# Kernel tuning notes

Hardware: AMD Instinct MI355X
Metric: run time of the kernel (lower is better)

Reference implementation:

```python
import jax, jax.numpy as jnp
import numpy as np

D_MODEL = 1024
EXPAND = 2
HEADDIM = 64
D_STATE = 128
D_CONV = 4
D_INNER = EXPAND * D_MODEL          # 2048
NHEADS = D_INNER // HEADDIM         # 32
CONV_DIM = D_INNER + 2 * D_STATE    # x, B, C share the depthwise conv
EPS = 1e-5


def setup_inputs() -> dict:
    key = jax.random.key(0)
    ks = jax.random.split(key, 8)
    d_in_proj = 2 * D_INNER + 2 * D_STATE + NHEADS
    x = jax.random.normal(ks[0], (2, 2048, D_MODEL), jnp.float32)
    W_in = jax.random.normal(ks[1], (D_MODEL, d_in_proj), jnp.float32) * (D_MODEL ** -0.5)
    conv_w = jax.random.normal(ks[2], (CONV_DIM, D_CONV), jnp.float32) * 0.2
    conv_b = jnp.zeros((CONV_DIM,), jnp.float32)
    # dt init: softplus(dt_bias) in [1e-3, 1e-1]  (inverse-softplus init, as in mamba_ssm)
    dt = jnp.exp(jax.random.uniform(ks[3], (NHEADS,), jnp.float32,
                                    minval=np.log(1e-3), maxval=np.log(1e-1)))
    dt_bias = dt + jnp.log(-jnp.expm1(-dt))
    A_log = jnp.log(jax.random.uniform(ks[4], (NHEADS,), jnp.float32, minval=1.0, maxval=16.0))
    D = jnp.ones((NHEADS,), jnp.float32)
    norm_w = jnp.ones((D_INNER,), jnp.float32)
    W_out = jax.random.normal(ks[5], (D_INNER, D_MODEL), jnp.float32) * (D_INNER ** -0.5)
    return dict(x=x, W_in=W_in, conv_w=conv_w, conv_b=conv_b, dt_bias=dt_bias,
                A_log=A_log, D=D, norm_w=norm_w, W_out=W_out)


def _causal_depthwise_conv(u, w, b):
    # u: (B, L, C), w: (C, K) depthwise, causal (pad K-1 on the left)
    B, L, C = u.shape
    up = jnp.pad(u, ((0, 0), (D_CONV - 1, 0), (0, 0)))
    y = b
    for k in range(D_CONV):
        y = y + up[:, k:k + L, :] * w[:, k]
    return y


def _rms(v):
    return v * jax.lax.rsqrt(jnp.mean(v * v, axis=-1, keepdims=True) + EPS)


def reference(x, W_in, conv_w, conv_b, dt_bias, A_log, D, norm_w, W_out):
    b, l, _ = x.shape
    zxbcdt = x @ W_in                                  # (b, l, 2*d_inner + 2*d_state + nheads)
    z = zxbcdt[..., :D_INNER]
    xBC = zxbcdt[..., D_INNER:D_INNER + CONV_DIM]
    dt = jax.nn.softplus(zxbcdt[..., -NHEADS:] + dt_bias)   # (b, l, h)
    xBC = jax.nn.silu(_causal_depthwise_conv(xBC, conv_w, conv_b))
    xs = xBC[..., :D_INNER].reshape(b, l, NHEADS, HEADDIM)  # (b, l, h, p)
    Bm = xBC[..., D_INNER:D_INNER + D_STATE]                 # (b, l, n)
    Cm = xBC[..., D_INNER + D_STATE:]                        # (b, l, n)
    A = -jnp.exp(A_log)                                      # (h,)
    decay = jnp.exp(dt * A)                                  # (b, l, h)

    def step(h, inp):
        dec_t, dt_t, x_t, B_t, C_t = inp   # (b,h) (b,h) (b,h,p) (b,n) (b,n)
        h = h * dec_t[:, :, None, None] + (dt_t[:, :, None] * x_t)[..., None] * B_t[:, None, None, :]
        y_t = jnp.einsum('bhpn,bn->bhp', h, C_t)
        return h, y_t

    h0 = jnp.zeros((b, NHEADS, HEADDIM, D_STATE), x.dtype)
    xs_t = (decay.transpose(1, 0, 2), dt.transpose(1, 0, 2),
            xs.transpose(1, 0, 2, 3), Bm.transpose(1, 0, 2), Cm.transpose(1, 0, 2))
    _, ys = jax.lax.scan(step, h0, xs_t)                     # ys: (l, b, h, p)
    y = ys.transpose(1, 0, 2, 3) + D[None, None, :, None] * xs
    y = y.reshape(b, l, D_INNER)
    # gated RMSNorm (RMSNormGated in mamba_ssm), then out projection
    y = _rms(y * jax.nn.silu(z)) * norm_w
    out = y @ W_out                                          # (b, l, d_model)
    # wrapper: post RMSNorm (weight freshly initialized to ones) + residual
    return _rms(out) + x
```

## Files before the change

### kernel.cpp

```cpp
#include <hip/hip_runtime.h>
#include <hip/hip_bf16.h>

#define DMODEL 1024
#define DI     2048
#define DSTATE 128
#define NH     32
#define HD     64
#define CONVD  2304
#define LSEQ   2048
#define BATCH  2
#define DPROJ  4384
#define NPAD   4480
#define EPSV   1e-5f
#define QCH    128
#define NCH    16

#define AS1 __attribute__((address_space(1)))
#define AS3 __attribute__((address_space(3)))

typedef __attribute__((ext_vector_type(8))) short bf16x8;
typedef __attribute__((ext_vector_type(4))) float f32x4;

union U4 { ushort4 u; __hip_bfloat16 h[4]; };

__device__ __forceinline__ float bf2f(unsigned short u) {
  union { unsigned int i; float f; } c; c.i = ((unsigned)u) << 16; return c.f;
}
__device__ __forceinline__ ushort4 pack4(float x0, float x1, float x2, float x3) {
  U4 p;
  p.h[0] = __float2bfloat16(x0); p.h[1] = __float2bfloat16(x1);
  p.h[2] = __float2bfloat16(x2); p.h[3] = __float2bfloat16(x3);
  return p.u;
}

__device__ __forceinline__ bf16x8 ldsfrag(const __hip_bfloat16* base, int row, int ke) {
  int byte = row * 256 + ke * 2;
  byte ^= (row & 7) << 4;
  return *reinterpret_cast<const bf16x8*>(reinterpret_cast<const char*>(base) + byte);
}
__device__ __forceinline__ void ldswr4(__hip_bfloat16* base, int row, int col, ushort4 v) {
  int byte = row * 256 + col * 2;
  byte ^= (row & 7) << 4;
  *reinterpret_cast<ushort4*>(reinterpret_cast<char*>(base) + byte) = v;
}
__device__ __forceinline__ ushort4 ldsrd4(const __hip_bfloat16* base, int row, int col) {
  int byte = row * 256 + col * 2;
  byte ^= (row & 7) << 4;
  return *reinterpret_cast<const ushort4*>(reinterpret_cast<const char*>(base) + byte);
}
__device__ __forceinline__ void ldswr8(__hip_bfloat16* base, int row, int colElem,
                                       unsigned lo, unsigned hi) {
  int byte = row * 256 + colElem * 2;
  byte ^= (row & 7) << 4;
  uint2 v; v.x = lo; v.y = hi;
  *reinterpret_cast<uint2*>(reinterpret_cast<char*>(base) + byte) = v;
}
__device__ __forceinline__ bf16x8 frag32(const __hip_bfloat16* base, int row, int g) {
  int byte = row * 64 + (((g ^ (row >> 1)) & 3) << 4);
  return *reinterpret_cast<const bf16x8*>(reinterpret_cast<const char*>(base) + byte);
}

__device__ __forceinline__ void quadtr(unsigned a01, unsigned a23, int ql,
                                       unsigned& w01, unsigned& w23) {
  unsigned y01 = __shfl_xor((int)a01, 1), y23 = __shfl_xor((int)a23, 1);
  unsigned c01 = (ql & 1) ? ((y01 >> 16) | (a01 & 0xFFFF0000u))
                          : ((a01 & 0xFFFFu) | (y01 << 16));
  unsigned c23 = (ql & 1) ? ((y23 >> 16) | (a23 & 0xFFFF0000u))
                          : ((a23 & 0xFFFFu) | (y23 << 16));
  unsigned d01 = __shfl_xor((int)c01, 2), d23 = __shfl_xor((int)c23, 2);
  w01 = (ql & 2) ? d23 : c01;
  w23 = (ql & 2) ? c23 : d01;
}


__global__ __launch_bounds__(256)
void prep_kernel(const float* __restrict__ x, __hip_bfloat16* __restrict__ xbf,
                 const float* __restrict__ W_in, __hip_bfloat16* __restrict__ wtin,
                 const float* __restrict__ W_out, __hip_bfloat16* __restrict__ wtout) {
  __shared__ float tile[32][33];
  const int b = blockIdx.x, tid = threadIdx.x;
  if (b < 4096) {
    int i = b * 256 + tid;
    float4 v = reinterpret_cast<const float4*>(x)[i];
    reinterpret_cast<ushort4*>(xbf)[i] = pack4(v.x, v.y, v.z, v.w);
    return;
  }
  const float* in;
  __hip_bfloat16* outp;
  int R, C, Cpad, n0, k0;
  if (b < 4096 + 4480) {
    int t = b - 4096;
    in = W_in; outp = wtin; R = 1024; C = 4384; Cpad = 4480;
    n0 = (t % 140) * 32; k0 = (t / 140) * 32;
  } else {
    int t = b - 8576;
    in = W_out; outp = wtout; R = 2048; C = 1024; Cpad = 1024;
    n0 = (t % 32) * 32; k0 = (t / 32) * 32;
  }
  int tx = tid & 31, ty = tid >> 5;
#pragma unroll
  for (int j = 0; j < 32; j += 8) {
    int k = k0 + ty + j, n = n0 + tx;
    tile[ty + j][tx] = (n < C) ? in[(size_t)k * C + n] : 0.f;
  }
  __syncthreads();
#pragma unroll
  for (int j = 0; j < 32; j += 8) {
    int n = n0 + ty + j, k = k0 + tx;
    if (n < Cpad) outp[(size_t)n * R + k] = __float2bfloat16(tile[tx][ty + j]);
  }
}


template <int MODE>
__global__ __launch_bounds__(512, 2)
void gemm256_bt(const __hip_bfloat16* __restrict__ A,
                const __hip_bfloat16* __restrict__ Bt,
                __hip_bfloat16* __restrict__ Cout,
                float* __restrict__ dtraw, int K) {
  __shared__ __hip_bfloat16 smA[4][256 * 32];
  __shared__ __hip_bfloat16 smB[4][256 * 32];

  int bm, bn, kbase, Kp;
  if constexpr (MODE == 0) {
    const int xcd = blockIdx.x & 7;
    const int i = blockIdx.x >> 3;
    bm = (xcd * 2 + (i & 1)) * 256;
    bn = (i >> 1) * 256;
    kbase = 0; Kp = K;
  } else {
    const int s = blockIdx.x >> 6;
    const int bb = blockIdx.x & 63;
    const int xcd = bb & 7;
    const int i = bb >> 3;
    bm = (xcd * 2 + (i & 1)) * 256;
    bn = (i >> 1) * 256;
    Kp = K >> 2; kbase = s * Kp;
  }
  const int tid = threadIdx.x;
  const int w = tid >> 6, lane = tid & 63;
  const int wm = w >> 2, wn = w & 3;
  const int fr = lane & 15, g = lane >> 4;
  const int srow = tid >> 2;
  const int sc = (((tid & 3) ^ ((srow >> 1) & 3)) << 3);

  f32x4 acc[8][4];
#pragma unroll
  for (int m = 0; m < 8; ++m)
#pragma unroll
    for (int n = 0; n < 4; ++n) acc[m][n] = (f32x4){0.f, 0.f, 0.f, 0.f};

  const __hip_bfloat16* aS = A + (size_t)(bm + srow) * K + kbase + sc;
  const __hip_bfloat16* bS = Bt + (size_t)(bn + srow) * K + kbase + sc;
  const int dbase = w * 512;

  auto STAGE = [&](int buf, int kt) {
    const int k0 = kt << 5;
#pragma unroll
    for (int j = 0; j < 2; ++j) {
      __builtin_amdgcn_global_load_lds((const AS1 void*)(aS + (size_t)(j * 128) * K + k0),
                                       (AS3 void*)(&smA[buf][j * 4096 + dbase]), 16, 0, 0);
      __builtin_amdgcn_global_load_lds((const AS1 void*)(bS + (size_t)(j * 128) * K + k0),
                                       (AS3 void*)(&smB[buf][j * 4096 + dbase]), 16, 0, 0);
    }
  };

  const int nt = Kp >> 5;
  STAGE(0, 0);
  STAGE(1, 1);
  for (int kt = 0; kt < nt; ++kt) {
    const int cur = kt & 3;
    if (kt + 2 < nt) {
      STAGE((kt + 2) & 3, kt + 2);
      asm volatile("s_waitcnt vmcnt(8)" ::: "memory");
    } else if (kt + 1 < nt) {
      asm volatile("s_waitcnt vmcnt(4)" ::: "memory");
    } else {
      asm volatile("s_waitcnt vmcnt(0)" ::: "memory");
    }
    __builtin_amdgcn_s_barrier();
    __builtin_amdgcn_s_setprio(1);
    bf16x8 af[8], bfv[4];
#pragma unroll
    for (int m = 0; m < 8; ++m)
      af[m] = frag32(&smA[cur][0], wm * 128 + m * 16 + fr, g);
#pragma unroll
    for (int n = 0; n < 4; ++n)
      bfv[n] = frag32(&smB[cur][0], wn * 64 + n * 16 + fr, g);
#pragma unroll
    for (int m = 0; m < 8; ++m)
#pragma unroll
      for (int n = 0; n < 4; ++n)
        acc[m][n] = __builtin_amdgcn_mfma_f32_16x16x32_bf16(af[m], bfv[n], acc[m][n], 0, 0, 0);
    __builtin_amdgcn_s_setprio(0);
  }

  const int rb = g * 4;
#pragma unroll
  for (int m = 0; m < 8; ++m)
#pragma unroll
    for (int n = 0; n < 4; ++n) {
      int row = bm + wm * 128 + m * 16 + rb;
      int col = bn + wn * 64 + n * 16 + fr;
      if constexpr (MODE == 0) {
        __hip_bfloat16* cp = Cout + (size_t)row * NPAD + col;
#pragma unroll
        for (int j = 0; j < 4; ++j)
          cp[(size_t)j * NPAD] = __float2bfloat16(acc[m][n][j]);
      } else {
        __hip_bfloat16* cp = Cout + (size_t)(blockIdx.x >> 6) * 4194304 +
                             (size_t)row * DMODEL + col;
#pragma unroll
        for (int j = 0; j < 4; ++j)
          cp[(size_t)j * DMODEL] = __float2bfloat16(acc[m][n][j]);
      }
    }

  if constexpr (MODE == 0) {
    const int bb = blockIdx.x;
    const int bm2 = (bb >> 3) * 128;
    const int bn2 = 4096 + (bb & 7) * 48;
    __hip_bfloat16* mA = &smA[0][0];
    __hip_bfloat16* mB = &smB[0][0];

    f32x4 ac2[3];
#pragma unroll
    for (int n = 0; n < 3; ++n) ac2[n] = (f32x4){0.f, 0.f, 0.f, 0.f};

    const __hip_bfloat16* aS2 = A + (size_t)(bm2 + srow) * K + sc;
    const __hip_bfloat16* bS2 = Bt + (size_t)(bn2 + srow) * K + sc;

    auto STG = [&](int buf, int kt) {
      const int k0 = kt << 5;
      __builtin_amdgcn_global_load_lds((const AS1 void*)(aS2 + k0),
                                       (AS3 void*)(&mA[buf * 4096 + dbase]), 16, 0, 0);
      if (w < 3)
        __builtin_amdgcn_global_load_lds((const AS1 void*)(bS2 + k0),
                                         (AS3 void*)(&mB[buf * 1536 + dbase]), 16, 0, 0);
    };

    const int nt2 = K >> 5;
    STG(0, 0);
    STG(1, 1);
    for (int kt = 0; kt < nt2; ++kt) {
      const int cur = kt & 3;
      if (kt + 2 < nt2) {
        STG((kt + 2) & 3, kt + 2);
        if (w < 3) { asm volatile("s_waitcnt vmcnt(4)" ::: "memory"); }
        else       { asm volatile("s_waitcnt vmcnt(2)" ::: "memory"); }
      } else if (kt + 1 < nt2) {
        if (w < 3) { asm volatile("s_waitcnt vmcnt(2)" ::: "memory"); }
        else       { asm volatile("s_waitcnt vmcnt(1)" ::: "memory"); }
      } else {
        asm volatile("s_waitcnt vmcnt(0)" ::: "memory");
      }
      __builtin_amdgcn_s_barrier();
      bf16x8 af = frag32(&mA[cur * 4096], w * 16 + fr, g);
      bf16x8 bfv[3];
#pragma unroll
      for (int n = 0; n < 3; ++n)
        bfv[n] = frag32(&mB[cur * 1536], n * 16 + fr, g);
#pragma unroll
      for (int n = 0; n < 3; ++n)
        ac2[n] = __builtin_amdgcn_mfma_f32_16x16x32_bf16(af, bfv[n], ac2[n], 0, 0, 0);
    }

#pragma unroll
    for (int n = 0; n < 3; ++n) {
      int row = bm2 + w * 16 + rb;
      int col = bn2 + n * 16 + fr;
      __hip_bfloat16* cp = Cout + (size_t)row * NPAD + col;
#pragma unroll
      for (int j = 0; j < 4; ++j) {
        float v = ac2[n][j];
        cp[(size_t)j * NPAD] = __float2bfloat16(v);
        if (col >= DI + CONVD && col < DPROJ)
          dtraw[(size_t)(row + j) * NH + (col - (DI + CONVD))] = v;
      }
    }
  }
}


__global__ __launch_bounds__(256)
void conv_stats_kernel(const __hip_bfloat16* __restrict__ zxb,
                       const float* __restrict__ cw,
                       const float* __restrict__ cb,
                       __hip_bfloat16* __restrict__ xbc,
                       const float* __restrict__ dtraw, const float* __restrict__ dt_bias,
                       const float* __restrict__ A_log,
                       float* __restrict__ csb, float* __restrict__ dtc,
                       float* __restrict__ swb, float* __restrict__ cumdecb,
                       float* __restrict__ pbuf) {
  if (blockIdx.x >= 1152) {
    int w = threadIdx.x >> 6, lane = threadIdx.x & 63;
    int bid = (blockIdx.x - 1152) * 4 + w;
    int c = bid & (NCH - 1);
    int h = (bid >> 4) & 31;
    int b = bid >> 9;
    int t0 = c * QCH;
    float a = expf(A_log[h]);
    float bias = dt_bias[h];
    const float* dtp = dtraw + ((size_t)b * LSEQ + t0) * NH + h;
    float r0 = dtp[lane * NH] + bias;
    float r1 = dtp[(64 + lane) * NH] + bias;
    float v0 = (r0 > 20.f) ? r0 : log1pf(expf(r0));
    float v1 = (r1 > 20.f) ? r1 : log1pf(expf(r1));
    float s0 = v0;
#pragma unroll
    for (int off = 1; off < 64; off <<= 1) {
      float tv = __shfl_up(s0, off);
      if (lane >= off) s0 += tv;
    }
    float T0 = __shfl(s0, 63);
    float s1 = v1;
#pragma unroll
    for (int off = 1; off < 64; off <<= 1) {
      float tv = __shfl_up(s1, off);
      if (lane >= off) s1 += tv;
    }
    float cs1 = s1 + T0;
    float Tt = __shfl(s1, 63) + T0;
    size_t base = (size_t)bid * 128;
    csb[base + lane] = s0;        csb[base + 64 + lane] = cs1;
    dtc[base + lane] = v0;        dtc[base + 64 + lane] = v1;
    swb[base + lane] = v0 * expf(-a * (Tt - s0));
    swb[base + 64 + lane] = v1 * expf(-a * (Tt - cs1));
    cumdecb[base + lane] = expf(-a * s0);
    cumdecb[base + 64 + lane] = expf(-a * cs1);
    if (lane == 0) pbuf[bid] = expf(-a * Tt);
    return;
  }
  int idx = blockIdx.x * 256 + threadIdx.x;
  int c4 = idx % (CONVD / 4);
  int bl8 = idx / (CONVD / 4);
  int l0 = (bl8 % (LSEQ / 8)) * 8;
  int b = bl8 / (LSEQ / 8);
  int c0 = c4 * 4;
  const __hip_bfloat16* src = zxb + (size_t)b * LSEQ * NPAD + DI + c0;

  float wv[4][4];
#pragma unroll
  for (int j = 0; j < 4; ++j)
    *reinterpret_cast<float4*>(wv[j]) = *reinterpret_cast<const float4*>(cw + (c0 + j) * 4);
  float bias[4];
  *reinterpret_cast<float4*>(bias) = *reinterpret_cast<const float4*>(cb + c0);

  float hist[11][4];
#pragma unroll
  for (int r = 0; r < 11; ++r) {
    int row = l0 - 3 + r;
    if (row >= 0) {
      ushort4 v = *reinterpret_cast<const ushort4*>(src + (size_t)row * NPAD);
      hist[r][0] = bf2f(v.x); hist[r][1] = bf2f(v.y);
      hist[r][2] = bf2f(v.z); hist[r][3] = bf2f(v.w);
    } else {
#pragma unroll
      for (int j = 0; j < 4; ++j) hist[r][j] = 0.f;
    }
  }

#pragma unroll
  for (int t = 0; t < 8; ++t) {
    float acc[4];
#pragma unroll
    for (int j = 0; j < 4; ++j) {
      float a = bias[j];
      a = fmaf(wv[j][0], hist[t + 0][j], a);
      a = fmaf(wv[j][1], hist[t + 1][j], a);
      a = fmaf(wv[j][2], hist[t + 2][j], a);
      a = fmaf(wv[j][3], hist[t + 3][j], a);
      acc[j] = a / (1.f + expf(-a));
    }
    *reinterpret_cast<ushort4*>(xbc + ((size_t)b * LSEQ + l0 + t) * CONVD + c0) =
        pack4(acc[0], acc[1], acc[2], acc[3]);
  }
}


__global__ __launch_bounds__(256, 2)
void ssd_mfma_local(const __hip_bfloat16* __restrict__ bxc,
                    const float* __restrict__ csb, const float* __restrict__ dtc,
                    const float* __restrict__ swb,
                    const float* __restrict__ A_log, const float* __restrict__ Dparm,
                    __hip_bfloat16* __restrict__ y, __hip_bfloat16* __restrict__ sbuf) {
  __shared__ __hip_bfloat16 T_B[128 * 128];
  __shared__ __hip_bfloat16 T_C[128 * 128];
  __shared__ __hip_bfloat16 T_X[64 * 128];

  const int bid = blockIdx.x;
  const int c = bid & (NCH - 1);
  const int h = (bid >> 4) & 31;
  const int b = bid >> 9;
  const int tid = threadIdx.x;
  const int w = tid >> 6, lane = tid & 63;
  const int q = lane >> 2, ql = lane & 3;
  const int t0 = c * QCH;
  const __hip_bfloat16* xc = bxc + (size_t)b * LSEQ * CONVD;
  const float a = expf(A_log[h]);
  const float Dh = Dparm[h];

  {
    const int rsub = lane >> 4;
    const int ch = lane & 15;
#pragma unroll
    for (int j = 0; j < 8; ++j) {
      int row = w * 32 + j * 4 + rsub;
      int sc_ = ch ^ (row & 7);
      const __hip_bfloat16* pB = xc + (size_t)(t0 + row) * CONVD + DI + sc_ * 8;
      __builtin_amdgcn_global_load_lds((const AS1 void*)pB,
                                       (AS3 void*)(T_B + (w * 32 + j * 4) * 128), 16, 0, 0);
      __builtin_amdgcn_global_load_lds((const AS1 void*)(pB + DSTATE),
                                       (AS3 void*)(T_C + (w * 32 + j * 4) * 128), 16, 0, 0);
    }
  }
#pragma unroll
  for (int r = 0; r < 8; ++r) {
    int gidx = w * 128 + q * 8 + r;
    int tb = (gidx & 31) * 4;
    int pb = (gidx >> 5) * 4;
    int t = tb + ql;
    ushort4 xv = *reinterpret_cast<const ushort4*>(xc + (size_t)(t0 + t) * CONVD + h * HD + pb);
    unsigned a01 = (unsigned)xv.x | ((unsigned)xv.y << 16);
    unsigned a23 = (unsigned)xv.z | ((unsigned)xv.w << 16);
    unsigned w01, w23;
    quadtr(a01, a23, ql, w01, w23);
    ldswr8(T_X, pb + ql, tb, w01, w23);
  }
  __syncthreads();

  const int fr = lane & 15;
  const int fk = (lane >> 4) * 8;
  const int rb = (lane >> 4) * 4;

  const int sR0 = (w >> 1) * 64, tC0 = (w & 1) * 64;
  f32x4 g[4][4];
#pragma unroll
  for (int m = 0; m < 4; ++m)
#pragma unroll
    for (int n = 0; n < 4; ++n) g[m][n] = (f32x4){0.f, 0.f, 0.f, 0.f};
  for (int kk = 0; kk < 128; kk += 32) {
    bf16x8 af[4], bfv[4];
#pragma unroll
    for (int m = 0; m < 4; ++m) af[m] = ldsfrag(T_B, sR0 + m * 16 + fr, kk + fk);
#pragma unroll
    for (int n = 0; n < 4; ++n) bfv[n] = ldsfrag(T_C, tC0 + n * 16 + fr, kk + fk);
#pragma unroll
    for (int m = 0; m < 4; ++m)
#pragma unroll
      for (int n = 0; n < 4; ++n)
        g[m][n] = __builtin_amdgcn_mfma_f32_16x16x32_bf16(af[m], bfv[n], g[m][n], 0, 0, 0);
  }
  __syncthreads();

  {
    const float* swp = swb + (size_t)bid * 128;
#pragma unroll
    for (int r = 0; r < 16; ++r) {
      int gidx = w * 256 + q * 16 + r;
      int tb = (gidx & 31) * 4;
      int nb = (gidx >> 5) * 4;
      int t = tb + ql;
      ushort4 bv = ldsrd4(T_B, t, nb);
      float wt = swp[t];
      ushort4 sv = pack4(bf2f(bv.x) * wt, bf2f(bv.y) * wt, bf2f(bv.z) * wt, bf2f(bv.w) * wt);
      unsigned a01 = (unsigned)sv.x | ((unsigned)sv.y << 16);
      unsigned a23 = (unsigned)sv.z | ((unsigned)sv.w << 16);
      unsigned w01, w23;
      quadtr(a01, a23, ql, w01, w23);
      ldswr8(T_C, nb + ql, tb, w01, w23);
    }
  }
  __syncthreads();

  {
    const float* csp = csb + (size_t)bid * 128;
    const float* dtp = dtc + (size_t)bid * 128;
#pragma unroll
    for (int m = 0; m < 4; ++m) {
      int sb0 = sR0 + m * 16 + rb;
      float cs_s[4], dt_s[4];
#pragma unroll
      for (int j = 0; j < 4; ++j) { cs_s[j] = csp[sb0 + j]; dt_s[j] = dtp[sb0 + j]; }
#pragma unroll
      for (int n = 0; n < 4; ++n) {
        int tt = tC0 + n * 16 + fr;
        float cst = csp[tt];
        float vv[4];
#pragma unroll
        for (int j = 0; j < 4; ++j) {
          int s = sb0 + j;
          float e = __expf(-a * (cst - cs_s[j])) * dt_s[j];
          float pv = (s <= tt) ? g[m][n][j] * e : 0.f;
          vv[j] = pv + ((s == tt) ? Dh : 0.f);
        }
        ldswr4(T_B, tt, sb0, pack4(vv[0], vv[1], vv[2], vv[3]));
      }
    }
  }
  __syncthreads();

  {
    int tR0 = w * 32;
    f32x4 yac[2][4];
#pragma unroll
    for (int m = 0; m < 2; ++m)
#pragma unroll
      for (int n = 0; n < 4; ++n) yac[m][n] = (f32x4){0.f, 0.f, 0.f, 0.f};
    for (int kk = 0; kk < 128; kk += 32) {
      bf16x8 af[2], bfv[4];
#pragma unroll
      for (int m = 0; m < 2; ++m) af[m] = ldsfrag(T_B, tR0 + m * 16 + fr, kk + fk);
#pragma unroll
      for (int n = 0; n < 4; ++n) bfv[n] = ldsfrag(T_X, n * 16 + fr, kk + fk);
#pragma unroll
      for (int m = 0; m < 2; ++m)
#pragma unroll
        for (int n = 0; n < 4; ++n)
          yac[m][n] = __builtin_amdgcn_mfma_f32_16x16x32_bf16(af[m], bfv[n], yac[m][n], 0, 0, 0);
    }
#pragma unroll
    for (int m = 0; m < 2; ++m)
#pragma unroll
      for (int n = 0; n < 4; ++n) {
        int trow = tR0 + m * 16 + rb;
        int pc = n * 16 + fr;
        __hip_bfloat16* yp = y + ((size_t)b * LSEQ + t0 + trow) * DI + h * HD + pc;
#pragma unroll
        for (int j = 0; j < 4; ++j)
          yp[(size_t)j * DI] = __float2bfloat16(yac[m][n][j]);
      }
  }

  {
    int pR0 = (w >> 1) * 32, nC0 = (w & 1) * 64;
    f32x4 sac[2][4];
#pragma unroll
    for (int m = 0; m < 2; ++m)
#pragma unroll
      for (int n = 0; n < 4; ++n) sac[m][n] = (f32x4){0.f, 0.f, 0.f, 0.f};
    for (int kk = 0; kk < 128; kk += 32) {
      bf16x8 af[2], bfv[4];
#pragma unroll
      for (int m = 0; m < 2; ++m) af[m] = ldsfrag(T_X, pR0 + m * 16 + fr, kk + fk);
#pragma unroll
      for (int n = 0; n < 4; ++n) bfv[n] = ldsfrag(T_C, nC0 + n * 16 + fr, kk + fk);
#pragma unroll
      for (int m = 0; m < 2; ++m)
#pragma unroll
        for (int n = 0; n < 4; ++n)
          sac[m][n] = __builtin_amdgcn_mfma_f32_16x16x32_bf16(af[m], bfv[n], sac[m][n], 0, 0, 0);
    }
    __hip_bfloat16* sg = sbuf + (size_t)bid * 8192;
#pragma unroll
    for (int m = 0; m < 2; ++m)
#pragma unroll
      for (int n = 0; n < 4; ++n) {
        int p = pR0 + m * 16 + rb;
        int nn = nC0 + n * 16 + fr;
#pragma unroll
        for (int j = 0; j < 4; ++j)
          sg[(size_t)(p + j) * 128 + nn] = __float2bfloat16(sac[m][n][j]);
      }
  }
}


__global__ void ssd_prop_kernel(__hip_bfloat16* __restrict__ sbuf,
                                const float* __restrict__ pbuf) {
  int idx = blockIdx.x * 256 + threadIdx.x;
  int bh = idx >> 13;
  int e = idx & 8191;
  __hip_bfloat16* base = sbuf + (size_t)bh * NCH * 8192 + e;
  const float* pb = pbuf + bh * NCH;
  float hs = 0.f;
  for (int cc = 0; cc < NCH; ++cc) {
    float sc = __bfloat162float(base[(size_t)cc * 8192]);
    base[(size_t)cc * 8192] = __float2bfloat16(hs);
    hs = fmaf(hs, pb[cc], sc);
  }
}


__global__ __launch_bounds__(256, 4)
void ssd_mfma_corr(const __hip_bfloat16* __restrict__ bxc, const __hip_bfloat16* __restrict__ sbuf,
                   const float* __restrict__ cumdecb, __hip_bfloat16* __restrict__ y) {
  const int bid = (blockIdx.x / 15) * 16 + 1 + (blockIdx.x % 15);
  const int h = (bid >> 4) & 31;
  const int b = bid >> 9;
  const int tid = threadIdx.x;
  const int w = tid >> 6, lane = tid & 63;
  const int t0 = (bid & (NCH - 1)) * QCH;
  const __hip_bfloat16* xc = bxc + (size_t)b * LSEQ * CONVD;
  const __hip_bfloat16* hsb = sbuf + (size_t)bid * 8192;
  const int fr = lane & 15;
  const int fk = (lane >> 4) * 8;
  const int rb = (lane >> 4) * 4;
  const int tR0 = w * 32;

  f32x4 ac[2][4];
#pragma unroll
  for (int m = 0; m < 2; ++m)
#pragma unroll
    for (int n = 0; n < 4; ++n) ac[m][n] = (f32x4){0.f, 0.f, 0.f, 0.f};

#pragma unroll
  for (int kk = 0; kk < 128; kk += 32) {
    bf16x8 af[2], bfv[4];
#pragma unroll
    for (int m = 0; m < 2; ++m)
      af[m] = *reinterpret_cast<const bf16x8*>(
          xc + (size_t)(t0 + tR0 + m * 16 + fr) * CONVD + DI + DSTATE + kk + fk);
#pragma unroll
    for (int n = 0; n < 4; ++n)
      bfv[n] = *reinterpret_cast<const bf16x8*>(hsb + (size_t)(n * 16 + fr) * 128 + kk + fk);
#pragma unroll
    for (int m = 0; m < 2; ++m)
#pragma unroll
      for (int n = 0; n < 4; ++n)
        ac[m][n] = __builtin_amdgcn_mfma_f32_16x16x32_bf16(af[m], bfv[n], ac[m][n], 0, 0, 0);
  }

  const float* cdp = cumdecb + (size_t)bid * 128;
#pragma unroll
  for (int m = 0; m < 2; ++m) {
    int trow = tR0 + m * 16 + rb;
    float cd[4];
#pragma unroll
    for (int j = 0; j < 4; ++j) cd[j] = cdp[trow + j];
#pragma unroll
    for (int n = 0; n < 4; ++n) {
      int pc = n * 16 + fr;
      __hip_bfloat16* yp = y + ((size_t)b * LSEQ + t0 + trow) * DI + h * HD + pc;
#pragma unroll
      for (int j = 0; j < 4; ++j) {
        float old = __bfloat162float(yp[(size_t)j * DI]);
        yp[(size_t)j * DI] = __float2bfloat16(old + cd[j] * ac[m][n][j]);
      }
    }
  }
}


__global__ __launch_bounds__(256)
void gate_rms_kernel(const __hip_bfloat16* __restrict__ y, const __hip_bfloat16* __restrict__ zxb,
                     const float* __restrict__ nw, __hip_bfloat16* __restrict__ g) {
  int row = blockIdx.x;
  int t = threadIdx.x;
  int c0 = t * 8;
  const __hip_bfloat16* yr = y + (size_t)row * DI + c0;
  const __hip_bfloat16* zr = zxb + (size_t)row * NPAD + c0;
  ushort4 y0 = *reinterpret_cast<const ushort4*>(yr);
  ushort4 y1 = *reinterpret_cast<const ushort4*>(yr + 4);
  ushort4 z0 = *reinterpret_cast<const ushort4*>(zr);
  ushort4 z1 = *reinterpret_cast<const ushort4*>(zr + 4);
  float zf[8] = {bf2f(z0.x), bf2f(z0.y), bf2f(z0.z), bf2f(z0.w),
                 bf2f(z1.x), bf2f(z1.y), bf2f(z1.z), bf2f(z1.w)};
  float yf[8] = {bf2f(y0.x), bf2f(y0.y), bf2f(y0.z), bf2f(y0.w),
                 bf2f(y1.x), bf2f(y1.y), bf2f(y1.z), bf2f(y1.w)};
  float v[8];
  float ss = 0.f;
#pragma unroll
  for (int j = 0; j < 8; ++j) {
    float z = zf[j];
    float vv = yf[j] * (z / (1.f + expf(-z)));
    v[j] = vv;
    ss += vv * vv;
  }
#pragma unroll
  for (int off = 32; off; off >>= 1) ss += __shfl_down(ss, off);
  __shared__ float red[4];
  if ((t & 63) == 0) red[t >> 6] = ss;
  __syncthreads();
  float tot = red[0] + red[1] + red[2] + red[3];
  float rstd = rsqrtf(tot * (1.f / DI) + EPSV);
  float4 na = *reinterpret_cast<const float4*>(nw + c0);
  float4 nb = *reinterpret_cast<const float4*>(nw + c0 + 4);
  ushort4 o0 = pack4(v[0] * rstd * na.x, v[1] * rstd * na.y,
                     v[2] * rstd * na.z, v[3] * rstd * na.w);
  ushort4 o1v = pack4(v[4] * rstd * nb.x, v[5] * rstd * nb.y,
                      v[6] * rstd * nb.z, v[7] * rstd * nb.w);
  ushort4* gp = reinterpret_cast<ushort4*>(g + (size_t)row * DI + c0);
  gp[0] = o0;
  gp[1] = o1v;
}


__global__ __launch_bounds__(256)
void final_rms_add(const __hip_bfloat16* __restrict__ o1p, const float* __restrict__ x,
                   float* __restrict__ out) {
  int row = blockIdx.x;
  int t = threadIdx.x;
  int c0 = t * 4;
  size_t off = (size_t)row * DMODEL + c0;
  float4 o = {0.f, 0.f, 0.f, 0.f};
#pragma unroll
  for (int s = 0; s < 4; ++s) {
    ushort4 p = *reinterpret_cast<const ushort4*>(o1p + (size_t)s * 4194304 + off);
    o.x += bf2f(p.x); o.y += bf2f(p.y); o.z += bf2f(p.z); o.w += bf2f(p.w);
  }
  float ss = o.x * o.x + o.y * o.y + o.z * o.z + o.w * o.w;
#pragma unroll
  for (int off2 = 32; off2; off2 >>= 1) ss += __shfl_down(ss, off2);
  __shared__ float red[4];
  if ((t & 63) == 0) red[t >> 6] = ss;
  __syncthreads();
  float tot = red[0] + red[1] + red[2] + red[3];
  float rstd = rsqrtf(tot * (1.f / DMODEL) + EPSV);
  float4 xv = *reinterpret_cast<const float4*>(x + off);
  float4 r;
  r.x = o.x * rstd + xv.x;
  r.y = o.y * rstd + xv.y;
  r.z = o.z * rstd + xv.z;
  r.w = o.w * rstd + xv.w;
  *reinterpret_cast<float4*>(out + off) = r;
}


extern "C" void kernel_launch(void* const* d_in, const int* in_sizes, int n_in,
                              void* d_out, int out_size, void* d_ws, size_t ws_size,
                              hipStream_t stream) {
  const float* x       = (const float*)d_in[0];
  const float* W_in    = (const float*)d_in[1];
  const float* conv_w  = (const float*)d_in[2];
  const float* conv_b  = (const float*)d_in[3];
  const float* dt_bias = (const float*)d_in[4];
  const float* A_log   = (const float*)d_in[5];
  const float* Dp      = (const float*)d_in[6];
  const float* norm_w  = (const float*)d_in[7];
  const float* W_out   = (const float*)d_in[8];
  float* out = (float*)d_out;

  float* zxF  = (float*)d_ws;
  __hip_bfloat16* zxb = (__hip_bfloat16*)zxF;
  __hip_bfloat16* o1p = zxb;
  float* xbcF = zxF + (size_t)18350080;
  __hip_bfloat16* xbc = (__hip_bfloat16*)xbcF;
  float* ybufF = xbcF + (size_t)9437184;
  __hip_bfloat16* ybuf = (__hip_bfloat16*)ybufF;
  float* dtraw = ybufF + (size_t)8388608;
  float* cumdecb = dtraw + (size_t)131072;
  __hip_bfloat16* xbf   = (__hip_bfloat16*)(cumdecb + 131072);
  __hip_bfloat16* wtin  = xbf + (size_t)4194304;
  __hip_bfloat16* wtout = wtin + (size_t)4587520;
  float* pbuf = (float*)(wtout + (size_t)2097152);
  float* csb  = pbuf + 1024;
  float* dtc  = csb + (size_t)131072;
  float* swb  = dtc + (size_t)131072;
  __hip_bfloat16* sbuf = xbf;
  __hip_bfloat16* gbf = xbf;

  prep_kernel<<<10624, 256, 0, stream>>>(x, xbf, W_in, wtin, W_out, wtout);

  gemm256_bt<0><<<256, 512, 0, stream>>>(xbf, wtin, zxb, dtraw, 1024);

  conv_stats_kernel<<<1408, 256, 0, stream>>>(zxb, conv_w, conv_b, xbc,
                                              dtraw, dt_bias, A_log,
                                              csb, dtc, swb, cumdecb, pbuf);

  ssd_mfma_local<<<1024, 256, 0, stream>>>(xbc, csb, dtc, swb, A_log, Dp, ybuf, sbuf);
  ssd_prop_kernel<<<2048, 256, 0, stream>>>(sbuf, pbuf);
  ssd_mfma_corr<<<960, 256, 0, stream>>>(xbc, sbuf, cumdecb, ybuf);

  gate_rms_kernel<<<4096, 256, 0, stream>>>(ybuf, zxb, norm_w, gbf);

  gemm256_bt<1><<<256, 512, 0, stream>>>(gbf, wtout, o1p, nullptr, 2048);

  final_rms_add<<<4096, 256, 0, stream>>>(o1p, x, out);
}
```

Baseline: 179.0 us.

## Fuse tail-column GEMM pass into main K loop reusing staged A tiles

The leftover 288 columns of the input projection were computed in a separate second K-loop after the main 256x256 tile, which reloaded A rows from global memory. They are now computed inside the main loop, reusing the A tile already in shared memory and staging only a small 48-column B slice per stage. This removes the second pass and its redundant A traffic. In exchange it adds extra shared memory and per-iteration loads and MFMAs, with wave-dependent vmcnt counts that must match exactly.

Result: faster. 172.3 us (-3.8%).

```diff
diff --git a/kernel.cpp b/kernel.cpp
--- a/kernel.cpp
+++ b/kernel.cpp
@@ -120,13 +120,16 @@
                 float* __restrict__ dtraw, int K) {
   __shared__ __hip_bfloat16 smA[4][256 * 32];
   __shared__ __hip_bfloat16 smB[4][256 * 32];
+  __shared__ __hip_bfloat16 smB2[4][48 * 32];
 
   int bm, bn, kbase, Kp;
+  int q2 = 0;
   if constexpr (MODE == 0) {
     const int xcd = blockIdx.x & 7;
     const int i = blockIdx.x >> 3;
     bm = (xcd * 2 + (i & 1)) * 256;
     bn = (i >> 1) * 256;
+    q2 = i >> 1;
     kbase = 0; Kp = K;
   } else {
     const int s = blockIdx.x >> 6;
@@ -143,15 +146,20 @@
   const int fr = lane & 15, g = lane >> 4;
   const int srow = tid >> 2;
   const int sc = (((tid & 3) ^ ((srow >> 1) & 3)) << 3);
+  const int rbase = (q2 & 1) * 128;
 
   f32x4 acc[8][4];
 #pragma unroll
   for (int m = 0; m < 8; ++m)
 #pragma unroll
     for (int n = 0; n < 4; ++n) acc[m][n] = (f32x4){0.f, 0.f, 0.f, 0.f};
+  f32x4 acc2[3];
+#pragma unroll
+  for (int n = 0; n < 3; ++n) acc2[n] = (f32x4){0.f, 0.f, 0.f, 0.f};
 
   const __hip_bfloat16* aS = A + (size_t)(bm + srow) * K + kbase + sc;
   const __hip_bfloat16* bS = Bt + (size_t)(bn + srow) * K + kbase + sc;
+  const __hip_bfloat16* bS2 = Bt + (size_t)(4096 + (q2 >> 1) * 48 + srow) * K + sc;
   const int dbase = w * 512;
 
   auto STAGE = [&](int buf, int kt) {
@@ -162,6 +170,11 @@
                                        (AS3 void*)(&smA[buf][j * 4096 + dbase]), 16, 0, 0);
       __builtin_amdgcn_global_load_lds((const AS1 void*)(bS + (size_t)(j * 128) * K + k0),
                                        (AS3 void*)(&smB[buf][j * 4096 + dbase]), 16, 0, 0);
+    }
+    if constexpr (MODE == 0) {
+      if (w < 3)
+        __builtin_amdgcn_global_load_lds((const AS1 void*)(bS2 + k0),
+                                         (AS3 void*)(&smB2[buf][dbase]), 16, 0, 0);
     }
   };
 
@@ -172,9 +185,19 @@
     const int cur = kt & 3;
     if (kt + 2 < nt) {
       STAGE((kt + 2) & 3, kt + 2);
-      asm volatile("s_waitcnt vmcnt(8)" ::: "memory");
+      if constexpr (MODE == 0) {
+        if (w < 3) { asm volatile("s_waitcnt vmcnt(10)" ::: "memory"); }
+        else       { asm volatile("s_waitcnt vmcnt(8)" ::: "memory"); }
+      } else {
+        asm volatile("s_waitcnt vmcnt(8)" ::: "memory");
+      }
     } else if (kt + 1 < nt) {
-      asm volatile("s_waitcnt vmcnt(4)" ::: "memory");
+      if constexpr (MODE == 0) {
+        if (w < 3) { asm volatile("s_waitcnt vmcnt(5)" ::: "memory"); }
+        else       { asm volatile("s_waitcnt vmcnt(4)" ::: "memory"); }
+      } else {
+        asm volatile("s_waitcnt vmcnt(4)" ::: "memory");
+      }
     } else {
       asm volatile("s_waitcnt vmcnt(0)" ::: "memory");
     }
@@ -192,6 +215,16 @@
 #pragma unroll
       for (int n = 0; n < 4; ++n)
         acc[m][n] = __builtin_amdgcn_mfma_f32_16x16x32_bf16(af[m], bfv[n], acc[m][n], 0, 0, 0);
+    if constexpr (MODE == 0) {
+      bf16x8 a2 = frag32(&smA[cur][0], rbase + w * 16 + fr, g);
+      bf16x8 b2[3];
+#pragma unroll
+      for (int n = 0; n < 3; ++n)
+        b2[n] = frag32(&smB2[cur][0], n * 16 + fr, g);
+#pragma unroll
+      for (int n = 0; n < 3; ++n)
+        acc2[n] = __builtin_amdgcn_mfma_f32_16x16x32_bf16(a2, b2[n], acc2[n], 0, 0, 0);
+    }
     __builtin_amdgcn_s_setprio(0);
   }
 
@@ -217,62 +250,15 @@
     }
 
   if constexpr (MODE == 0) {
-    const int bb = blockIdx.x;
-    const int bm2 = (bb >> 3) * 128;
-    const int bn2 = 4096 + (bb & 7) * 48;
-    __hip_bfloat16* mA = &smA[0][0];
-    __hip_bfloat16* mB = &smB[0][0];
-
-    f32x4 ac2[3];
-#pragma unroll
-    for (int n = 0; n < 3; ++n) ac2[n] = (f32x4){0.f, 0.f, 0.f, 0.f};
-
-    const __hip_bfloat16* aS2 = A + (size_t)(bm2 + srow) * K + sc;
-    const __hip_bfloat16* bS2 = Bt + (size_t)(bn2 + srow) * K + sc;
-
-    auto STG = [&](int buf, int kt) {
-      const int k0 = kt << 5;
-      __builtin_amdgcn_global_load_lds((const AS1 void*)(aS2 + k0),
-                                       (AS3 void*)(&mA[buf * 4096 + dbase]), 16, 0, 0);
-      if (w < 3)
-        __builtin_amdgcn_global_load_lds((const AS1 void*)(bS2 + k0),
-                                         (AS3 void*)(&mB[buf * 1536 + dbase]), 16, 0, 0);
-    };
-
-    const int nt2 = K >> 5;
-    STG(0, 0);
-    STG(1, 1);
-    for (int kt = 0; kt < nt2; ++kt) {
-      const int cur = kt & 3;
-      if (kt + 2 < nt2) {
-        STG((kt + 2) & 3, kt + 2);
-        if (w < 3) { asm volatile("s_waitcnt vmcnt(4)" ::: "memory"); }
-        else       { asm volatile("s_waitcnt vmcnt(2)" ::: "memory"); }
-      } else if (kt + 1 < nt2) {
-        if (w < 3) { asm volatile("s_waitcnt vmcnt(2)" ::: "memory"); }
-        else       { asm volatile("s_waitcnt vmcnt(1)" ::: "memory"); }
-      } else {
-        asm volatile("s_waitcnt vmcnt(0)" ::: "memory");
-      }
-      __builtin_amdgcn_s_barrier();
-      bf16x8 af = frag32(&mA[cur * 4096], w * 16 + fr, g);
-      bf16x8 bfv[3];
-#pragma unroll
-      for (int n = 0; n < 3; ++n)
-        bfv[n] = frag32(&mB[cur * 1536], n * 16 + fr, g);
-#pragma unroll
-      for (int n = 0; n < 3; ++n)
-        ac2[n] = __builtin_amdgcn_mfma_f32_16x16x32_bf16(af, bfv[n], ac2[n], 0, 0, 0);
-    }
-
+    const int bn2 = 4096 + (q2 >> 1) * 48;
 #pragma unroll
     for (int n = 0; n < 3; ++n) {
-      int row = bm2 + w * 16 + rb;
+      int row = bm + rbase + w * 16 + rb;
       int col = bn2 + n * 16 + fr;
       __hip_bfloat16* cp = Cout + (size_t)row * NPAD + col;
 #pragma unroll
       for (int j = 0; j < 4; ++j) {
-        float v = ac2[n][j];
+        float v = acc2[n][j];
         cp[(size_t)j * NPAD] = __float2bfloat16(v);
         if (col >= DI + CONVD && col < DPROJ)
           dtraw[(size_t)(row + j) * NH + (col - (DI + CONVD))] = v;
```
